# Optimization experiments

Hardware: AMD Instinct MI355X
Metric: run time of the kernel (lower is better)

## Reference

```python
import jax, jax.numpy as jnp
import numpy as np

B, T, H, W, C = 2, 8, 64, 64, 128
NH, KT, KH, KW = 4, 3, 7, 7
HD = C // NH
SCALE = HD ** -0.5


def _starts(L, ks):
    i = jnp.arange(L)
    return jnp.clip(i - ks // 2, 0, L - ks)  # NATTEN border-clamped window start


def _na3d(q, k, v, rpb):
    # q,k,v: [B,T,H,W,NH,HD]; rpb: [NH,2KT-1,2KH-1,2KW-1]
    st, sh, sw = _starts(T, KT), _starts(H, KH), _starts(W, KW)
    ot, oh, ow = jnp.meshgrid(jnp.arange(KT), jnp.arange(KH), jnp.arange(KW), indexing='ij')
    ot, oh, ow = ot.ravel(), oh.ravel(), ow.ravel()          # [K] kernel offsets, K=KT*KH*KW
    t_abs = st[None, :] + ot[:, None]                        # [K,T] absolute neighbor coords
    h_abs = sh[None, :] + oh[:, None]                        # [K,H]
    w_abs = sw[None, :] + ow[:, None]                        # [K,W]
    qs = q * SCALE
    it, ih, iw = jnp.arange(T), jnp.arange(H), jnp.arange(W)

    def score_step(_, idx):
        ta, ha, wa = idx
        kg = k[:, ta][:, :, ha][:, :, :, wa]                 # [B,T,H,W,NH,HD] shifted keys
        s = jnp.einsum('bthwnd,bthwnd->bthwn', qs, kg)
        rt = ta - it + (KT - 1)
        rh = ha - ih + (KH - 1)
        rw = wa - iw + (KW - 1)
        bias = rpb[:, rt][:, :, rh][:, :, :, rw]             # [NH,T,H,W]
        return None, s + jnp.transpose(bias, (1, 2, 3, 0))[None]

    _, scores = jax.lax.scan(score_step, None, (t_abs, h_abs, w_abs))  # [K,B,T,H,W,NH]
    attn = jax.nn.softmax(scores, axis=0)

    def av_step(acc, xs):
        a, ta, ha, wa = xs
        vg = v[:, ta][:, :, ha][:, :, :, wa]                 # [B,T,H,W,NH,HD]
        return acc + a[..., None] * vg, None

    out, _ = jax.lax.scan(av_step, jnp.zeros_like(q), (attn, t_abs, h_abs, w_abs))
    return out


def setup_inputs() -> dict:
    key = jax.random.key(0)
    ks = jax.random.split(key, 6)
    x = jax.random.normal(ks[0], (B, T, H, W, C), jnp.float32)
    y = jax.random.normal(ks[1], (B, T, H, W, C), jnp.float32)
    qv_w = jax.random.normal(ks[2], (C, 2 * C), jnp.float32) * 0.02
    qv_b = jnp.zeros((2 * C,), jnp.float32)
    k_w = jax.random.normal(ks[3], (C, C), jnp.float32) * 0.02
    k_b = jnp.zeros((C,), jnp.float32)
    proj_w = jax.random.normal(ks[4], (C, C), jnp.float32) * 0.02
    proj_b = jnp.zeros((C,), jnp.float32)
    rpb = jax.random.normal(ks[5], (NH, 2 * KT - 1, 2 * KH - 1, 2 * KW - 1), jnp.float32) * 0.02
    return {'x': x, 'y': y, 'qv_w': qv_w, 'qv_b': qv_b, 'k_w': k_w, 'k_b': k_b,
            'proj_w': proj_w, 'proj_b': proj_b, 'rpb': rpb}


def reference(x, y, qv_w, qv_b, k_w, k_b, proj_w, proj_b, rpb):
    qv = (x @ qv_w + qv_b).reshape(B, T, H, W, 2, NH, HD)
    q, v = qv[..., 0, :, :], qv[..., 1, :, :]
    k = (y @ k_w + k_b).reshape(B, T, H, W, NH, HD)
    o = _na3d(q, k, v, rpb).reshape(B, T, H, W, C)
    return o @ proj_w + proj_b
```

## Files before the change

### kernel.cpp

```cpp
#include <hip/hip_runtime.h>
#include <hip/hip_bf16.h>
#include <hip/hip_fp16.h>
#include <cmath>

#define Bv   2
#define Tv   8
#define Hv   64
#define Wv   64
#define MPOS (Bv*Tv*Hv*Wv)
#define SCALEv 0.17677669529663687f

#define SPOS  196
#define SVT   464
#define NCOLS 232

#define KOFF   0
#define VTOFF  13312
#define POFF   28160
#define RPBOFF 57856
#define INVOFF 61248
#define SMEM_BYTES 61504

#define KPAD 136

typedef __attribute__((ext_vector_type(8))) short bf16x8;
typedef __attribute__((ext_vector_type(4))) float f32x4;

__device__ __forceinline__ unsigned short f2bf16(float x) {
  return __builtin_bit_cast(unsigned short, __float2bfloat16(x));
}
__device__ __forceinline__ float bf2f(unsigned short h) {
  return __uint_as_float((unsigned)h << 16);
}
__device__ __forceinline__ float h2f(unsigned short h) {
  return __half2float(__builtin_bit_cast(__half, h));
}
__device__ __forceinline__ unsigned short f2h(float x) {
  return __builtin_bit_cast(unsigned short, __float2half(x));
}
__device__ __forceinline__ unsigned pk2(float a, float b) {
  return (unsigned)f2bf16(a) | ((unsigned)f2bf16(b) << 16);
}
__device__ __forceinline__ void gload_lds16(const void* gsrc, void* ldst) {
  __builtin_amdgcn_global_load_lds(
      (const __attribute__((address_space(1))) unsigned int*)gsrc,
      (__attribute__((address_space(3))) unsigned int*)ldst, 16, 0, 0);
}

__global__ __launch_bounds__(256) void preconvert(
    const float* __restrict__ qv_w, const float* __restrict__ k_w,
    const float* __restrict__ proj_w,
    ushort* __restrict__ wqvT, ushort* __restrict__ wkT,
    ushort* __restrict__ wpT_hi, ushort* __restrict__ wpT_lo) {
  const int id = blockIdx.x * 256 + threadIdx.x;
  if (id < 32768) {
    const int n = id >> 7, kk = id & 127;
    wqvT[n * KPAD + kk] = f2bf16(qv_w[kk * 256 + n]);
  } else if (id < 49152) {
    const int j = id - 32768;
    const int n = j >> 7, kk = j & 127;
    wkT[n * KPAD + kk] = f2bf16(k_w[kk * 128 + n]);
  } else {
    const int j = id - 49152;
    const int n = j >> 7, kk = j & 127;
    const float v = proj_w[kk * 128 + n];
    const unsigned short hi = f2bf16(v);
    wpT_hi[n * KPAD + kk] = hi;
    wpT_lo[n * KPAD + kk] = f2bf16(v - bf2f(hi));
  }
}

__global__ __launch_bounds__(512) void gemm_qvk(
    const float* __restrict__ x, const float* __restrict__ y,
    const ushort* __restrict__ wqvT, const ushort* __restrict__ wkT,
    const float* __restrict__ qv_b, const float* __restrict__ k_b,
    ushort* __restrict__ qbuf, ushort* __restrict__ vbuf,
    ushort* __restrict__ kbuf) {
  __shared__ ushort Ws[128 * KPAD];
  const int tid  = threadIdx.x;
  const int bx   = blockIdx.x;
  const int seg  = bx >> 9;
  const int row0 = (bx & 511) * 128;

  const float*  A    = (seg == 2) ? y : x;
  const ushort* W    = (seg == 0) ? wqvT : (seg == 1) ? wqvT + 128 * KPAD : wkT;
  const float*  bias = (seg == 0) ? qv_b : (seg == 1) ? qv_b + 128 : k_b;
  ushort*       outp = (seg == 0) ? qbuf : (seg == 1) ? vbuf : kbuf;
  const float   scale = (seg == 0) ? SCALEv : 1.0f;

  {
    const uint4* wg = (const uint4*)W;
    for (int i = tid; i < 2176; i += 512)
      gload_lds16(wg + i, (uint4*)Ws + i);
  }

  const int wv = tid >> 6, lane = tid & 63, quad = lane >> 4, l16 = lane & 15;
  const int arow = row0 + wv * 16 + l16;

  bf16x8 af[4];
#pragma unroll
  for (int kk = 0; kk < 4; ++kk) {
    const float4* ap = (const float4*)(A + (size_t)arow * 128 + kk * 32 + quad * 8);
    const float4 a = ap[0], b2 = ap[1];
    af[kk] = __builtin_bit_cast(bf16x8,
        make_uint4(pk2(a.x, a.y), pk2(a.z, a.w), pk2(b2.x, b2.y), pk2(b2.z, b2.w)));
  }
  __syncthreads();

  f32x4 C[8];
#pragma unroll
  for (int nt = 0; nt < 8; ++nt) C[nt] = (f32x4){0.f, 0.f, 0.f, 0.f};

#pragma unroll
  for (int kk = 0; kk < 4; ++kk) {
#pragma unroll
    for (int nt = 0; nt < 8; ++nt) {
      const bf16x8 b2 = *(const bf16x8*)(Ws + (nt * 16 + l16) * KPAD + kk * 32 + quad * 8);
      C[nt] = __builtin_amdgcn_mfma_f32_16x16x32_bf16(af[kk], b2, C[nt], 0, 0, 0);
    }
  }

#pragma unroll
  for (int nt = 0; nt < 8; ++nt) {
    const int col = nt * 16 + l16;
    const float bv = bias[col];
#pragma unroll
    for (int r2 = 0; r2 < 4; ++r2) {
      const size_t row = row0 + wv * 16 + quad * 4 + r2;
      outp[(size_t)(col >> 5) * MPOS * 32 + row * 32 + (col & 31)] =
          f2bf16((C[nt][r2] + bv) * scale);
    }
  }
}

__global__ __launch_bounds__(512) void gemm_proj_mfma(
    const float* __restrict__ o, const ushort* __restrict__ wpT_hi,
    const ushort* __restrict__ wpT_lo, const float* __restrict__ proj_b,
    float* __restrict__ out) {
  __shared__ ushort Wh[128 * KPAD];
  __shared__ ushort Wl[128 * KPAD];
  const int tid  = threadIdx.x;
  const int row0 = blockIdx.x * 128;
  {
    const uint4* wgh = (const uint4*)wpT_hi;
    const uint4* wgl = (const uint4*)wpT_lo;
    for (int i = tid; i < 2176; i += 512) {
      gload_lds16(wgh + i, (uint4*)Wh + i);
      gload_lds16(wgl + i, (uint4*)Wl + i);
    }
  }

  const int wv = tid >> 6, lane = tid & 63, quad = lane >> 4, l16 = lane & 15;
  const int arow = row0 + wv * 16 + l16;

  bf16x8 ah[4], al[4];
#pragma unroll
  for (int kk = 0; kk < 4; ++kk) {
    const float4* ap =
        (const float4*)(o + (size_t)kk * MPOS * 32 + (size_t)arow * 32 + quad * 8);
    const float4 a = ap[0], b2 = ap[1];
    const float vs[8] = {a.x, a.y, a.z, a.w, b2.x, b2.y, b2.z, b2.w};
    unsigned hw[4], lw[4];
#pragma unroll
    for (int e = 0; e < 4; ++e) {
      const unsigned short h0 = f2bf16(vs[2 * e]);
      const unsigned short h1 = f2bf16(vs[2 * e + 1]);
      hw[e] = (unsigned)h0 | ((unsigned)h1 << 16);
      lw[e] = (unsigned)f2bf16(vs[2 * e] - bf2f(h0)) |
              ((unsigned)f2bf16(vs[2 * e + 1] - bf2f(h1)) << 16);
    }
    ah[kk] = __builtin_bit_cast(bf16x8, make_uint4(hw[0], hw[1], hw[2], hw[3]));
    al[kk] = __builtin_bit_cast(bf16x8, make_uint4(lw[0], lw[1], lw[2], lw[3]));
  }
  __syncthreads();

  f32x4 C[8];
#pragma unroll
  for (int nt = 0; nt < 8; ++nt) C[nt] = (f32x4){0.f, 0.f, 0.f, 0.f};

#pragma unroll
  for (int kk = 0; kk < 4; ++kk) {
#pragma unroll
    for (int nt = 0; nt < 8; ++nt) {
      const int boff = (nt * 16 + l16) * KPAD + kk * 32 + quad * 8;
      const bf16x8 bh = *(const bf16x8*)(Wh + boff);
      const bf16x8 bl = *(const bf16x8*)(Wl + boff);
      C[nt] = __builtin_amdgcn_mfma_f32_16x16x32_bf16(ah[kk], bh, C[nt], 0, 0, 0);
      C[nt] = __builtin_amdgcn_mfma_f32_16x16x32_bf16(ah[kk], bl, C[nt], 0, 0, 0);
      C[nt] = __builtin_amdgcn_mfma_f32_16x16x32_bf16(al[kk], bh, C[nt], 0, 0, 0);
    }
  }

#pragma unroll
  for (int nt = 0; nt < 8; ++nt) {
    const int col = nt * 16 + l16;
    const float bv = proj_b[col];
#pragma unroll
    for (int r2 = 0; r2 < 4; ++r2) {
      const size_t row = row0 + wv * 16 + quad * 4 + r2;
      out[row * 128 + col] = C[nt][r2] + bv;
    }
  }
}

__global__ __launch_bounds__(512, 4)
void na3d_tile(
    const ushort* __restrict__ qin,
    const ushort* __restrict__ kin,
    const ushort* __restrict__ vin,
    const float* __restrict__ rpb,
    float* __restrict__ oout) {
  __shared__ __align__(16) unsigned char smem[SMEM_BYTES];

  const int tid  = threadIdx.x;
  const int wv   = tid >> 6;
  const int lane = tid & 63;
  const int quad = lane >> 4;
  const int l16  = lane & 15;

  const int bx   = blockIdx.x;
  const int head = bx & 3;
  const int tile = bx >> 2;
  const int w0 = (tile & 7) << 3;
  const int h0 = ((tile >> 3) & 7) << 3;
  const int t  = (tile >> 6) & 7;
  const int b  = tile >> 9;

  const int st  = min(max(t - 1, 0), Tv - 3);
  const int u_h = min(max(h0 - 3, 0), Hv - 14);
  const int u_w = min(max(w0 - 3, 0), Wv - 14);
  const int rt_b = st - t + 2;

  const ushort* qin_h = qin + (size_t)head * MPOS * 32;
  const uint4*  kin_h = (const uint4*)kin + (size_t)head * MPOS * 4;
  const uint4*  vin_h = (const uint4*)vin + (size_t)head * MPOS * 4;

  const int mtile = wv & 3;
  bf16x8 afrag;
  {
    const int q_a  = mtile * 16 + l16;
    const int qh_a = h0 + (q_a >> 3), qw_a = w0 + (q_a & 7);
    const size_t qpos_a = ((size_t)(b * Tv + t) * Hv + qh_a) * Wv + qw_a;
    afrag = *(const bf16x8*)(qin_h + qpos_a * 32 + quad * 8);
  }
  {
    float r0 = 0.f, r1 = 0.f;
    if (tid < 845) r0 = rpb[head * 845 + tid];
    if (tid < 333) r1 = rpb[head * 845 + tid + 512];
    if (tid < 845) ((float*)(smem + RPBOFF))[tid] = r0;
    if (tid < 333) ((float*)(smem + RPBOFF))[tid + 512] = r1;
  }

  const int qs = tid >> 3, l8s = tid & 7;
  const int qh_s = h0 + (qs >> 3), qw_s = w0 + (qs & 7);
  const int sh_s = min(max(qh_s - 3, 0), Hv - 7);
  const int sw_s = min(max(qw_s - 3, 0), Wv - 7);
  const int dh_s = sh_s - u_h, dw_s = sw_s - u_w;
  const int rh0 = sh_s - qh_s + 6, rw0 = sw_s - qw_s + 6;

  const int mtA = wv >> 1, ntA = wv & 1;
  const int dcol = ntA * 16 + l16;
  const unsigned vsw = ((unsigned)(dcol >> 3) & 3u) << 5;

  f32x4 o = {0.f, 0.f, 0.f, 0.f};
  float sum = 0.f;
  uint4 vv0, vv1;

  const int vp0 = tid >> 2, vc0 = tid & 3;
  const int vr0 = vp0 / 14;
  const unsigned vsp0 = ((u_h + vr0) * Wv + (u_w + (vp0 - vr0 * 14))) * 4 + vc0;
  const int j1 = tid + 512;
  const int vp1 = j1 >> 2, vc1 = j1 & 3;
  const int vr1 = vp1 / 14;
  const unsigned vsp1 = ((u_h + vr1) * Wv + (u_w + (vp1 - vr1 * 14))) * 4 + vc1;

  {
    const unsigned tbase = (unsigned)(b * Tv + st) * (Hv * Wv * 4);
    vv0 = vin_h[tbase + vsp0];
    if (tid < 272) vv1 = vin_h[tbase + vsp1];
    for (int ch = wv; ch < 13; ch += 8) {
      const int m = ch * 64 + lane;
      const int pos = min(m >> 2, SPOS - 1);
      const int c = ((m & 3) - (pos >> 2)) & 3;
      const int rh = pos / 14;
      const unsigned sp = ((u_h + rh) * Wv + (u_w + (pos - rh * 14))) * 4 + c;
      gload_lds16(kin_h + tbase + sp, smem + KOFF + ch * 1024 + lane * 16);
    }
  }

#pragma unroll 1
  for (int pass = 0; pass < 3; ++pass) {
    {
      const unsigned sw0 = (unsigned)vc0 << 5;
      const unsigned v4[4] = {vv0.x, vv0.y, vv0.z, vv0.w};
#pragma unroll
      for (int m2 = 0; m2 < 4; ++m2) {
        const int d0 = 8 * vc0 + 2 * m2;
        const unsigned base = (unsigned)d0 * SVT + (unsigned)vp0 * 2;
        *(ushort*)(smem + VTOFF + (base ^ sw0))         = (ushort)(v4[m2] & 0xffffu);
        *(ushort*)(smem + VTOFF + ((base + SVT) ^ sw0)) = (ushort)(v4[m2] >> 16);
      }
      if (tid < 272) {
        const unsigned sw1 = (unsigned)vc1 << 5;
        const unsigned w4[4] = {vv1.x, vv1.y, vv1.z, vv1.w};
#pragma unroll
        for (int m2 = 0; m2 < 4; ++m2) {
          const int d0 = 8 * vc1 + 2 * m2;
          const unsigned base = (unsigned)d0 * SVT + (unsigned)vp1 * 2;
          *(ushort*)(smem + VTOFF + (base ^ sw1))         = (ushort)(w4[m2] & 0xffffu);
          *(ushort*)(smem + VTOFF + ((base + SVT) ^ sw1)) = (ushort)(w4[m2] >> 16);
        }
      }
    }
    if (pass == 0) {
      for (int i = tid; i < 576; i += 512) {
        const int d = i / 18, jj = i - d * 18;
        const unsigned base = (unsigned)d * SVT + 392u + (unsigned)jj * 4;
        *(unsigned*)(smem + VTOFF + (base ^ (((unsigned)d >> 3) << 5))) = 0u;
      }
    }
    __syncthreads();

    {
      ushort* ph = (ushort*)(smem + POFF);
      for (int nt = (wv >> 2); nt < 13; nt += 2) {
        const int u = nt * 16 + l16;
        const int slot = (quad + (u >> 2)) & 3;
        const bf16x8 bfrag = *(const bf16x8*)(smem + KOFF + u * 64 + slot * 16);
        f32x4 c = {0.f, 0.f, 0.f, 0.f};
        c = __builtin_amdgcn_mfma_f32_16x16x32_bf16(afrag, bfrag, c, 0, 0, 0);
#pragma unroll
        for (int r2 = 0; r2 < 4; ++r2) {
          const int qrow = mtile * 16 + quad * 4 + r2;
          ph[qrow * NCOLS + u] = f2h(c[r2]);
        }
      }
    }
    __syncthreads();

    {
      const ushort* Ps = (const ushort*)(smem + POFF) + qs * NCOLS;
      const float* rpb_l = (const float*)(smem + RPBOFF) + (rt_b + pass) * 169;
      float ex[7];
      int uu[7];
#pragma unroll
      for (int k = 0; k < 7; ++k) {
        const int e = l8s + 8 * k;
        const int a = (e * 37) >> 8;
        const int bb = e - 7 * a;
        uu[k] = (dh_s + a) * 14 + dw_s + bb;
        if (e < 49) {
          const float s = h2f(Ps[uu[k]]) + rpb_l[(rh0 + a) * 13 + rw0 + bb];
          ex[k] = __expf(s);
          sum += ex[k];
        }
      }
      if (pass == 2) {
        float sm = sum;
        sm += __shfl_xor(sm, 1);
        sm += __shfl_xor(sm, 2);
        sm += __shfl_xor(sm, 4);
        if (l8s == 0) ((float*)(smem + INVOFF))[qs] = 1.0f / sm;
      }
      __builtin_amdgcn_sched_barrier(0);
      {
        uint4* Pv = (uint4*)(smem + POFF + (size_t)qs * SVT);
#pragma unroll
        for (int c = 0; c < 4; ++c) {
          const int idx = l8s + 8 * c;
          if (idx < 29) Pv[idx] = make_uint4(0u, 0u, 0u, 0u);
        }
      }
      __builtin_amdgcn_sched_barrier(0);
      ushort* Pr = (ushort*)(smem + POFF) + qs * NCOLS;
#pragma unroll
      for (int k = 0; k < 7; ++k) {
        const int e = l8s + 8 * k;
        if (e < 49) Pr[uu[k]] = f2bf16(ex[k]);
      }
    }
    __syncthreads();

    if (pass < 2) {
      const unsigned tbase = (unsigned)(b * Tv + st + pass + 1) * (Hv * Wv * 4);
      vv0 = vin_h[tbase + vsp0];
      if (tid < 272) vv1 = vin_h[tbase + vsp1];
      for (int ch = wv; ch < 13; ch += 8) {
        const int m = ch * 64 + lane;
        const int pos = min(m >> 2, SPOS - 1);
        const int c = ((m & 3) - (pos >> 2)) & 3;
        const int rh = pos / 14;
        const unsigned sp = ((u_h + rh) * Wv + (u_w + (pos - rh * 14))) * 4 + c;
        gload_lds16(kin_h + tbase + sp, smem + KOFF + ch * 1024 + lane * 16);
      }
    }

    {
      const unsigned char* Abase = smem + POFF + (size_t)(mtA * 16 + l16) * SVT;
      const unsigned vlocal = (unsigned)dcol * SVT;
#pragma unroll
      for (int kt = 0; kt < 7; ++kt) {
        const bf16x8 a  = *(const bf16x8*)(Abase + kt * 64 + quad * 16);
        const bf16x8 bb = *(const bf16x8*)(smem + VTOFF +
                            ((vlocal + kt * 64 + quad * 16) ^ vsw));
        o = __builtin_amdgcn_mfma_f32_16x16x32_bf16(a, bb, o, 0, 0, 0);
      }
    }
    if (pass < 2) __syncthreads();
  }

  {
    float* oout_h = oout + (size_t)head * MPOS * 32;
    const float* invArr = (const float*)(smem + INVOFF);
#pragma unroll
    for (int r2 = 0; r2 < 4; ++r2) {
      const int qrow = mtA * 16 + quad * 4 + r2;
      const float val = o[r2] * invArr[qrow];
      const int qh2 = h0 + (qrow >> 3), qw2 = w0 + (qrow & 7);
      const size_t qp2 = ((size_t)(b * Tv + t) * Hv + qh2) * Wv + qw2;
      oout_h[qp2 * 32 + dcol] = val;
    }
  }
}

extern "C" void kernel_launch(void* const* d_in, const int* in_sizes, int n_in,
                              void* d_out, int out_size, void* d_ws, size_t ws_size,
                              hipStream_t stream) {
  const float* x      = (const float*)d_in[0];
  const float* y      = (const float*)d_in[1];
  const float* qv_w   = (const float*)d_in[2];
  const float* qv_b   = (const float*)d_in[3];
  const float* k_w    = (const float*)d_in[4];
  const float* k_b    = (const float*)d_in[5];
  const float* proj_w = (const float*)d_in[6];
  const float* proj_b = (const float*)d_in[7];
  const float* rpb    = (const float*)d_in[8];
  float* out = (float*)d_out;

  const size_t elems = (size_t)MPOS * 128;
  ushort* qbuf = (ushort*)d_ws;
  ushort* kbuf = qbuf + elems;
  ushort* vbuf = kbuf + elems;
  float*  obuf = (float*)(vbuf + elems);
  ushort* wqvT   = (ushort*)(obuf + elems);
  ushort* wkT    = wqvT + 256 * KPAD;
  ushort* wpT_hi = wkT + 128 * KPAD;
  ushort* wpT_lo = wpT_hi + 128 * KPAD;

  preconvert    <<<256,  256, 0, stream>>>(qv_w, k_w, proj_w, wqvT, wkT, wpT_hi, wpT_lo);
  gemm_qvk      <<<1536, 512, 0, stream>>>(x, y, wqvT, wkT, qv_b, k_b, qbuf, vbuf, kbuf);
  na3d_tile     <<<4096, 512, 0, stream>>>(qbuf, kbuf, vbuf, rpb, obuf);
  gemm_proj_mfma<<<512,  512, 0, stream>>>(obuf, wpT_hi, wpT_lo, proj_b, out);
}
```

Before: 242.3 us.

## Store V transposed in GEMM epilogue and double-buffer V tiles via direct LDS loads

New measurement: 241.7 us. Within noise of the previous version (-0.2%).

```diff
diff --git a/kernel.cpp b/kernel.cpp
--- a/kernel.cpp
+++ b/kernel.cpp
@@ -10,16 +10,16 @@
 #define MPOS (Bv*Tv*Hv*Wv)
 #define SCALEv 0.17677669529663687f
 
-#define SPOS  196
 #define SVT   464
 #define NCOLS 232
 
 #define KOFF   0
-#define VTOFF  13312
-#define POFF   28160
-#define RPBOFF 57856
-#define INVOFF 61248
-#define SMEM_BYTES 61504
+#define VT0    14336
+#define VT1    30720
+#define POFF   47104
+#define RPBOFF 76800
+#define INVOFF 80180
+#define SMEM_BYTES 80448
 
 #define KPAD 136
 
@@ -85,7 +85,6 @@
   const float*  A    = (seg == 2) ? y : x;
   const ushort* W    = (seg == 0) ? wqvT : (seg == 1) ? wqvT + 128 * KPAD : wkT;
   const float*  bias = (seg == 0) ? qv_b : (seg == 1) ? qv_b + 128 : k_b;
-  ushort*       outp = (seg == 0) ? qbuf : (seg == 1) ? vbuf : kbuf;
   const float   scale = (seg == 0) ? SCALEv : 1.0f;
 
   {
@@ -120,15 +119,30 @@
     }
   }
 
-#pragma unroll
-  for (int nt = 0; nt < 8; ++nt) {
-    const int col = nt * 16 + l16;
-    const float bv = bias[col];
-#pragma unroll
-    for (int r2 = 0; r2 < 4; ++r2) {
-      const size_t row = row0 + wv * 16 + quad * 4 + r2;
-      outp[(size_t)(col >> 5) * MPOS * 32 + row * 32 + (col & 31)] =
-          f2bf16((C[nt][r2] + bv) * scale);
+  if (seg == 1) {
+    const int p0 = row0 + wv * 16 + quad * 4;
+    const int bt = p0 >> 12, sp = p0 & 4095;
+#pragma unroll
+    for (int nt = 0; nt < 8; ++nt) {
+      const int d = nt * 16 + l16;
+      const float bv = bias[d];
+      const ushort4 pk4 = make_ushort4(
+          f2bf16(C[nt][0] + bv), f2bf16(C[nt][1] + bv),
+          f2bf16(C[nt][2] + bv), f2bf16(C[nt][3] + bv));
+      *(ushort4*)(vbuf + (size_t)(((d >> 5) * 16 + bt) * 32 + (d & 31)) * 4096 + sp) = pk4;
+    }
+  } else {
+    ushort* outp = (seg == 0) ? qbuf : kbuf;
+#pragma unroll
+    for (int nt = 0; nt < 8; ++nt) {
+      const int col = nt * 16 + l16;
+      const float bv = bias[col];
+#pragma unroll
+      for (int r2 = 0; r2 < 4; ++r2) {
+        const size_t row = row0 + wv * 16 + quad * 4 + r2;
+        outp[(size_t)(col >> 5) * MPOS * 32 + row * 32 + (col & 31)] =
+            f2bf16((C[nt][r2] + bv) * scale);
+      }
     }
   }
 }
@@ -233,7 +247,6 @@
 
   const ushort* qin_h = qin + (size_t)head * MPOS * 32;
   const uint4*  kin_h = (const uint4*)kin + (size_t)head * MPOS * 4;
-  const uint4*  vin_h = (const uint4*)vin + (size_t)head * MPOS * 4;
 
   const int mtile = wv & 3;
   bf16x8 afrag;
@@ -260,70 +273,49 @@
 
   const int mtA = wv >> 1, ntA = wv & 1;
   const int dcol = ntA * 16 + l16;
-  const unsigned vsw = ((unsigned)(dcol >> 3) & 3u) << 5;
+  const unsigned vbase = (unsigned)dcol * 512;
+  const unsigned vsw = ((unsigned)dcol & 7u) << 4;
+
+  unsigned ksp[2]; int kch[2]; int nk = 0;
+  for (int ch = wv; ch < 14; ch += 8) {
+    const int m = ch * 64 + lane;
+    const int pos = m >> 2;
+    const int c = ((m & 3) - (pos >> 2)) & 3;
+    const int rh = pos >> 4, rw = min(pos & 15, 13);
+    ksp[nk] = ((u_h + rh) * Wv + (u_w + rw)) * 4 + c;
+    kch[nk] = ch;
+    ++nk;
+  }
+  unsigned vofs[2];
+#pragma unroll
+  for (int it = 0; it < 2; ++it) {
+    const int i = tid + it * 512;
+    const int d = i >> 5;
+    const int blk = (i & 31) ^ (d & 7);
+    const int rh = blk >> 1, rw0b = (blk & 1) << 3;
+    vofs[it] = (unsigned)d * 4096 + (u_h + rh) * 64 + (u_w + rw0b);
+  }
 
   f32x4 o = {0.f, 0.f, 0.f, 0.f};
   float sum = 0.f;
-  uint4 vv0, vv1;
-
-  const int vp0 = tid >> 2, vc0 = tid & 3;
-  const int vr0 = vp0 / 14;
-  const unsigned vsp0 = ((u_h + vr0) * Wv + (u_w + (vp0 - vr0 * 14))) * 4 + vc0;
-  const int j1 = tid + 512;
-  const int vp1 = j1 >> 2, vc1 = j1 & 3;
-  const int vr1 = vp1 / 14;
-  const unsigned vsp1 = ((u_h + vr1) * Wv + (u_w + (vp1 - vr1 * 14))) * 4 + vc1;
-
-  {
-    const unsigned tbase = (unsigned)(b * Tv + st) * (Hv * Wv * 4);
-    vv0 = vin_h[tbase + vsp0];
-    if (tid < 272) vv1 = vin_h[tbase + vsp1];
-    for (int ch = wv; ch < 13; ch += 8) {
-      const int m = ch * 64 + lane;
-      const int pos = min(m >> 2, SPOS - 1);
-      const int c = ((m & 3) - (pos >> 2)) & 3;
-      const int rh = pos / 14;
-      const unsigned sp = ((u_h + rh) * Wv + (u_w + (pos - rh * 14))) * 4 + c;
-      gload_lds16(kin_h + tbase + sp, smem + KOFF + ch * 1024 + lane * 16);
-    }
+
+  {
+    const unsigned tb_k = (unsigned)(b * Tv + st) * (Hv * Wv * 4);
+    for (int s = 0; s < nk; ++s)
+      gload_lds16(kin_h + tb_k + ksp[s], smem + KOFF + kch[s] * 1024 + lane * 16);
+    const ushort* vpl = vin + (size_t)(head * 16 + b * Tv + st) * 32 * 4096;
+#pragma unroll
+    for (int it = 0; it < 2; ++it)
+      gload_lds16(vpl + vofs[it], smem + VT0 + (tid + it * 512) * 16);
   }
 
 #pragma unroll 1
   for (int pass = 0; pass < 3; ++pass) {
-    {
-      const unsigned sw0 = (unsigned)vc0 << 5;
-      const unsigned v4[4] = {vv0.x, vv0.y, vv0.z, vv0.w};
-#pragma unroll
-      for (int m2 = 0; m2 < 4; ++m2) {
-        const int d0 = 8 * vc0 + 2 * m2;
-        const unsigned base = (unsigned)d0 * SVT + (unsigned)vp0 * 2;
-        *(ushort*)(smem + VTOFF + (base ^ sw0))         = (ushort)(v4[m2] & 0xffffu);
-        *(ushort*)(smem + VTOFF + ((base + SVT) ^ sw0)) = (ushort)(v4[m2] >> 16);
-      }
-      if (tid < 272) {
-        const unsigned sw1 = (unsigned)vc1 << 5;
-        const unsigned w4[4] = {vv1.x, vv1.y, vv1.z, vv1.w};
-#pragma unroll
-        for (int m2 = 0; m2 < 4; ++m2) {
-          const int d0 = 8 * vc1 + 2 * m2;
-          const unsigned base = (unsigned)d0 * SVT + (unsigned)vp1 * 2;
-          *(ushort*)(smem + VTOFF + (base ^ sw1))         = (ushort)(w4[m2] & 0xffffu);
-          *(ushort*)(smem + VTOFF + ((base + SVT) ^ sw1)) = (ushort)(w4[m2] >> 16);
-        }
-      }
-    }
-    if (pass == 0) {
-      for (int i = tid; i < 576; i += 512) {
-        const int d = i / 18, jj = i - d * 18;
-        const unsigned base = (unsigned)d * SVT + 392u + (unsigned)jj * 4;
-        *(unsigned*)(smem + VTOFF + (base ^ (((unsigned)d >> 3) << 5))) = 0u;
-      }
-    }
     __syncthreads();
 
     {
       ushort* ph = (ushort*)(smem + POFF);
-      for (int nt = (wv >> 2); nt < 13; nt += 2) {
+      for (int nt = (wv >> 2); nt < 14; nt += 2) {
         const int u = nt * 16 + l16;
         const int slot = (quad + (u >> 2)) & 3;
         const bf16x8 bfrag = *(const bf16x8*)(smem + KOFF + u * 64 + slot * 16);
@@ -338,6 +330,18 @@
     }
     __syncthreads();
 
+    if (pass < 2) {
+      const unsigned tb_k = (unsigned)(b * Tv + st + pass + 1) * (Hv * Wv * 4);
+      for (int s = 0; s < nk; ++s)
+        gload_lds16(kin_h + tb_k + ksp[s], smem + KOFF + kch[s] * 1024 + lane * 16);
+      const ushort* vpl =
+          vin + (size_t)(head * 16 + b * Tv + st + pass + 1) * 32 * 4096;
+      const unsigned vtn = ((pass + 1) & 1) ? VT1 : VT0;
+#pragma unroll
+      for (int it = 0; it < 2; ++it)
+        gload_lds16(vpl + vofs[it], smem + vtn + (tid + it * 512) * 16);
+    }
+
     {
       const ushort* Ps = (const ushort*)(smem + POFF) + qs * NCOLS;
       const float* rpb_l = (const float*)(smem + RPBOFF) + (rt_b + pass) * 169;
@@ -348,7 +352,7 @@
         const int e = l8s + 8 * k;
         const int a = (e * 37) >> 8;
         const int bb = e - 7 * a;
-        uu[k] = (dh_s + a) * 14 + dw_s + bb;
+        uu[k] = (dh_s + a) * 16 + dw_s + bb;
         if (e < 49) {
           const float s = h2f(Ps[uu[k]]) + rpb_l[(rh0 + a) * 13 + rw0 + bb];
           ex[k] = __expf(s);
@@ -381,32 +385,17 @@
     }
     __syncthreads();
 
-    if (pass < 2) {
-      const unsigned tbase = (unsigned)(b * Tv + st + pass + 1) * (Hv * Wv * 4);
-      vv0 = vin_h[tbase + vsp0];
-      if (tid < 272) vv1 = vin_h[tbase + vsp1];
-      for (int ch = wv; ch < 13; ch += 8) {
-        const int m = ch * 64 + lane;
-        const int pos = min(m >> 2, SPOS - 1);
-        const int c = ((m & 3) - (pos >> 2)) & 3;
-        const int rh = pos / 14;
-        const unsigned sp = ((u_h + rh) * Wv + (u_w + (pos - rh * 14))) * 4 + c;
-        gload_lds16(kin_h + tbase + sp, smem + KOFF + ch * 1024 + lane * 16);
-      }
-    }
-
     {
+      const unsigned vt = (pass & 1) ? VT1 : VT0;
       const unsigned char* Abase = smem + POFF + (size_t)(mtA * 16 + l16) * SVT;
-      const unsigned vlocal = (unsigned)dcol * SVT;
 #pragma unroll
       for (int kt = 0; kt < 7; ++kt) {
         const bf16x8 a  = *(const bf16x8*)(Abase + kt * 64 + quad * 16);
-        const bf16x8 bb = *(const bf16x8*)(smem + VTOFF +
-                            ((vlocal + kt * 64 + quad * 16) ^ vsw));
+        const bf16x8 bb = *(const bf16x8*)(smem + vt +
+                            ((vbase + kt * 64 + quad * 16) ^ vsw));
         o = __builtin_amdgcn_mfma_f32_16x16x32_bf16(a, bb, o, 0, 0, 0);
       }
     }
-    if (pass < 2) __syncthreads();
   }
 
   {
```
